# Kernel tuning notes

Measured on AMD Instinct MI355X. Metric: run time of the kernel, lower is better.

The kernel has to match this reference:

```python
import jax, jax.numpy as jnp
import numpy as np

KERNEL_SIZE = 7
STRIDE = 1
PADDING = 3
DILATION = 1
PAD_MODE = 1  # 1 -> reflection pad, 0 -> zero pad (SAN convention)


def setup_inputs() -> dict:
    key = jax.random.key(0)
    x = jax.random.normal(key, (8, 64, 56, 56), dtype=jnp.float32)
    return {"input_": x}


def _subtraction(x, k, stride, padding, dilation, pad_mode):
    B, C, H, W = x.shape
    Hout = (H + 2 * padding - dilation * (k - 1) - 1) // stride + 1
    Wout = (W + 2 * padding - dilation * (k - 1) - 1) // stride + 1
    mode = "reflect" if pad_mode == 1 else "constant"
    xp = jnp.pad(x, ((0, 0), (0, 0), (padding, padding), (padding, padding)), mode=mode)
    # center: 1x1 unfold of the UNPADDED input with the same stride -> [B,C,Hout,Wout]
    center = x[:, :, ::stride, ::stride][:, :, :Hout, :Wout]
    # neighborhood: k*k shifted strided views of the padded input (no big im2col copy per-view)
    h_span = (Hout - 1) * stride + 1
    w_span = (Wout - 1) * stride + 1
    patches = []
    for i in range(k):
        for j in range(k):
            patches.append(
                xp[:, :,
                   i * dilation : i * dilation + h_span : stride,
                   j * dilation : j * dilation + w_span : stride]
            )
    nb = jnp.stack(patches, axis=2)  # [B, C, k*k, Hout, Wout]
    out = center[:, :, None, :, :] - nb  # broadcast subtract center vs neighborhood
    return out.reshape(B, C, k * k, Hout * Wout)


def reference(input_):
    return _subtraction(input_, KERNEL_SIZE, STRIDE, PADDING, DILATION, PAD_MODE)
```

## Files before the change

### kernel.cpp

```cpp
#include <hip/hip_runtime.h>

#define HH 56
#define WW 56
#define HWOUT (HH * WW)
#define NBC (8 * 64)
#define NBLK (NBC * 7)
#define NXCD 8
#define CPX (NBLK / NXCD)

typedef float f32x4 __attribute__((ext_vector_type(4)));

__device__ __forceinline__ int refl(int t) {
    t = (t < 0) ? -t : t;
    return (t >= HH) ? (2 * HH - 2 - t) : t;
}

__global__ __launch_bounds__(256) void sub_kernel(const float* __restrict__ x,
                                                  float* __restrict__ out) {
    const int bid = blockIdx.x;
    const int blk = (bid % NXCD) * CPX + bid / NXCD;

    const int di = blk % 7;
    const int bc = blk / 7;

    const float* __restrict__ img = x + (size_t)bc * HWOUT;
    float* __restrict__ oplane0 = out + ((size_t)bc * 49 + (size_t)di * 7) * HWOUT;

    for (int q = threadIdx.x; q < HWOUT / 4; q += 256) {
        const int e = q * 4;
        const int h = e / WW;
        const int w = e - h * WW;

        const float* __restrict__ crow = img + h * WW;
        const float* __restrict__ nrow = img + refl(h + di - 3) * WW;

        const f32x4 cen = *reinterpret_cast<const f32x4*>(crow + w);

        float wnd[12];
        {
            const f32x4 lo = *reinterpret_cast<const f32x4*>(nrow + (w == 0 ? 0 : w - 4));
            wnd[0] = lo.x; wnd[1] = lo.y; wnd[2] = lo.z; wnd[3] = lo.w;
        }
        {
            const f32x4 mid = *reinterpret_cast<const f32x4*>(nrow + w);
            wnd[4] = mid.x; wnd[5] = mid.y; wnd[6] = mid.z; wnd[7] = mid.w;
        }
        {
            const f32x4 hi = *reinterpret_cast<const f32x4*>(nrow + (w == 52 ? 48 : w + 4));
            wnd[8] = hi.x; wnd[9] = hi.y; wnd[10] = hi.z; wnd[11] = hi.w;
        }
        if (w == 0) {
            wnd[1] = nrow[3]; wnd[2] = nrow[2]; wnd[3] = nrow[1];
        }
        if (w == 52) {
            wnd[8] = nrow[54]; wnd[9] = nrow[53]; wnd[10] = nrow[52];
        }

        float* __restrict__ op = oplane0 + e;
        #pragma unroll
        for (int djj = 0; djj < 7; ++djj) {
            f32x4 r;
            r.x = cen.x - wnd[djj + 1];
            r.y = cen.y - wnd[djj + 2];
            r.z = cen.z - wnd[djj + 3];
            r.w = cen.w - wnd[djj + 4];
            *reinterpret_cast<f32x4*>(op + (size_t)djj * HWOUT) = r;
        }
    }
}

extern "C" void kernel_launch(void* const* d_in, const int* in_sizes, int n_in,
                              void* d_out, int out_size, void* d_ws, size_t ws_size,
                              hipStream_t stream) {
    const float* x = (const float*)d_in[0];
    float* out = (float*)d_out;
    sub_kernel<<<dim3(NBLK), dim3(256), 0, stream>>>(x, out);
}
```

Baseline: 60.88 us.

## Software-pipeline window loads across unrolled iterations and drop XCD block remap

Replaces the strided loop with a fully unrolled sequence in which the next iteration's input loads are issued before the current iteration's stores, so load latency overlaps with writes. Reflection-edge fixups now reuse values already held in the middle vector instead of issuing extra scalar global loads. The XCD-aware block index remapping is removed, so blocks map directly to planes. This raises register pressure and may change L2 locality across XCDs.

```diff
diff --git a/kernel.cpp b/kernel.cpp
--- a/kernel.cpp
+++ b/kernel.cpp
@@ -3,10 +3,7 @@
 #define HH 56
 #define WW 56
 #define HWOUT (HH * WW)
-#define NBC (8 * 64)
-#define NBLK (NBC * 7)
-#define NXCD 8
-#define CPX (NBLK / NXCD)
+#define NBLK (8 * 64 * 7)
 
 typedef float f32x4 __attribute__((ext_vector_type(4)));
 
@@ -15,58 +12,66 @@
     return (t >= HH) ? (2 * HH - 2 - t) : t;
 }
 
+__device__ __forceinline__ void load_win(const float* __restrict__ img, int di, int q,
+                                         f32x4& cen, f32x4& lo, f32x4& mid, f32x4& hi,
+                                         int& w_out) {
+    const int e = q * 4;
+    const int h = e / WW;
+    const int w = e - h * WW;
+    const float* crow = img + h * WW;
+    const float* nrow = img + refl(h + di - 3) * WW;
+    cen = *reinterpret_cast<const f32x4*>(crow + w);
+    lo  = *reinterpret_cast<const f32x4*>(nrow + (w == 0 ? 0 : w - 4));
+    mid = *reinterpret_cast<const f32x4*>(nrow + w);
+    hi  = *reinterpret_cast<const f32x4*>(nrow + (w == 52 ? 48 : w + 4));
+    w_out = w;
+}
+
+__device__ __forceinline__ void finish(float* __restrict__ oplane0, int q, int w,
+                                       f32x4 cen, f32x4 lo, f32x4 mid, f32x4 hi) {
+    float wnd[12];
+    wnd[0] = lo.x;  wnd[1] = lo.y;  wnd[2] = lo.z;  wnd[3] = lo.w;
+    wnd[4] = mid.x; wnd[5] = mid.y; wnd[6] = mid.z; wnd[7] = mid.w;
+    wnd[8] = hi.x;  wnd[9] = hi.y;  wnd[10] = hi.z; wnd[11] = hi.w;
+    if (w == 0)  { wnd[1] = mid.w; wnd[2] = mid.z; wnd[3] = mid.y; }
+    if (w == 52) { wnd[8] = mid.z; wnd[9] = mid.y; wnd[10] = mid.x; }
+
+    float* __restrict__ op = oplane0 + q * 4;
+    #pragma unroll
+    for (int djj = 0; djj < 7; ++djj) {
+        f32x4 r;
+        r.x = cen.x - wnd[djj + 1];
+        r.y = cen.y - wnd[djj + 2];
+        r.z = cen.z - wnd[djj + 3];
+        r.w = cen.w - wnd[djj + 4];
+        *reinterpret_cast<f32x4*>(op + (size_t)djj * HWOUT) = r;
+    }
+}
+
 __global__ __launch_bounds__(256) void sub_kernel(const float* __restrict__ x,
                                                   float* __restrict__ out) {
-    const int bid = blockIdx.x;
-    const int blk = (bid % NXCD) * CPX + bid / NXCD;
-
+    const int blk = blockIdx.x;
     const int di = blk % 7;
     const int bc = blk / 7;
+    const int tid = threadIdx.x;
 
     const float* __restrict__ img = x + (size_t)bc * HWOUT;
     float* __restrict__ oplane0 = out + ((size_t)bc * 49 + (size_t)di * 7) * HWOUT;
 
-    for (int q = threadIdx.x; q < HWOUT / 4; q += 256) {
-        const int e = q * 4;
-        const int h = e / WW;
-        const int w = e - h * WW;
+    f32x4 c0, l0, m0, h0; int w0;
+    f32x4 c1, l1, m1, h1; int w1;
+    f32x4 c2, l2, m2, h2; int w2;
+    f32x4 c3, l3, m3, h3; int w3;
+    const bool tail = (tid < 784 - 768);
 
-        const float* __restrict__ crow = img + h * WW;
-        const float* __restrict__ nrow = img + refl(h + di - 3) * WW;
-
-        const f32x4 cen = *reinterpret_cast<const f32x4*>(crow + w);
-
-        float wnd[12];
-        {
-            const f32x4 lo = *reinterpret_cast<const f32x4*>(nrow + (w == 0 ? 0 : w - 4));
-            wnd[0] = lo.x; wnd[1] = lo.y; wnd[2] = lo.z; wnd[3] = lo.w;
-        }
-        {
-            const f32x4 mid = *reinterpret_cast<const f32x4*>(nrow + w);
-            wnd[4] = mid.x; wnd[5] = mid.y; wnd[6] = mid.z; wnd[7] = mid.w;
-        }
-        {
-            const f32x4 hi = *reinterpret_cast<const f32x4*>(nrow + (w == 52 ? 48 : w + 4));
-            wnd[8] = hi.x; wnd[9] = hi.y; wnd[10] = hi.z; wnd[11] = hi.w;
-        }
-        if (w == 0) {
-            wnd[1] = nrow[3]; wnd[2] = nrow[2]; wnd[3] = nrow[1];
-        }
-        if (w == 52) {
-            wnd[8] = nrow[54]; wnd[9] = nrow[53]; wnd[10] = nrow[52];
-        }
-
-        float* __restrict__ op = oplane0 + e;
-        #pragma unroll
-        for (int djj = 0; djj < 7; ++djj) {
-            f32x4 r;
-            r.x = cen.x - wnd[djj + 1];
-            r.y = cen.y - wnd[djj + 2];
-            r.z = cen.z - wnd[djj + 3];
-            r.w = cen.w - wnd[djj + 4];
-            *reinterpret_cast<f32x4*>(op + (size_t)djj * HWOUT) = r;
-        }
-    }
+    load_win(img, di, tid,       c0, l0, m0, h0, w0);
+    load_win(img, di, tid + 256, c1, l1, m1, h1, w1);
+    finish(oplane0, tid, w0, c0, l0, m0, h0);
+    load_win(img, di, tid + 512, c2, l2, m2, h2, w2);
+    finish(oplane0, tid + 256, w1, c1, l1, m1, h1);
+    if (tail) load_win(img, di, tid + 768, c3, l3, m3, h3, w3);
+    finish(oplane0, tid + 512, w2, c2, l2, m2, h2);
+    if (tail) finish(oplane0, tid + 768, w3, c3, l3, m3, h3);
 }
 
 extern "C" void kernel_launch(void* const* d_in, const int* in_sizes, int n_in,
```

After: 57.60 us. 1.06x faster.

## Stage each channel plane in LDS and loop all row offsets per block

Applied to the files above, without the earlier changes.

Launches one block per (batch, channel) plane instead of seven, loading the plane into shared memory once and reusing it for all seven row offsets. Reflection edge values are taken from the already loaded middle vector rather than extra loads. This aims to cut redundant global reads of the input, but it reduces the grid to 512 blocks and drops the XCD-aware block remapping, which may lower occupancy and store throughput for a write-bound kernel.

```diff
diff --git a/kernel.cpp b/kernel.cpp
--- a/kernel.cpp
+++ b/kernel.cpp
@@ -4,9 +4,6 @@
 #define WW 56
 #define HWOUT (HH * WW)
 #define NBC (8 * 64)
-#define NBLK (NBC * 7)
-#define NXCD 8
-#define CPX (NBLK / NXCD)
 
 typedef float f32x4 __attribute__((ext_vector_type(4)));
 
@@ -17,54 +14,51 @@
 
 __global__ __launch_bounds__(256) void sub_kernel(const float* __restrict__ x,
                                                   float* __restrict__ out) {
-    const int bid = blockIdx.x;
-    const int blk = (bid % NXCD) * CPX + bid / NXCD;
+    __shared__ float img[HWOUT];
+    const int bc = blockIdx.x;
+    const int tid = threadIdx.x;
 
-    const int di = blk % 7;
-    const int bc = blk / 7;
+    const float* __restrict__ gimg = x + (size_t)bc * HWOUT;
+    for (int q = tid; q < HWOUT / 4; q += 256) {
+        *reinterpret_cast<f32x4*>(&img[q * 4]) =
+            *reinterpret_cast<const f32x4*>(gimg + q * 4);
+    }
+    __syncthreads();
 
-    const float* __restrict__ img = x + (size_t)bc * HWOUT;
-    float* __restrict__ oplane0 = out + ((size_t)bc * 49 + (size_t)di * 7) * HWOUT;
+    float* __restrict__ obase = out + (size_t)bc * 49 * HWOUT;
 
-    for (int q = threadIdx.x; q < HWOUT / 4; q += 256) {
-        const int e = q * 4;
-        const int h = e / WW;
-        const int w = e - h * WW;
+    for (int di = 0; di < 7; ++di) {
+        float* __restrict__ oplane0 = obase + (size_t)di * 7 * HWOUT;
+        for (int q = tid; q < HWOUT / 4; q += 256) {
+            const int e = q * 4;
+            const int h = e / WW;
+            const int w = e - h * WW;
 
-        const float* __restrict__ crow = img + h * WW;
-        const float* __restrict__ nrow = img + refl(h + di - 3) * WW;
+            const float* crow = &img[h * WW];
+            const float* nrow = &img[refl(h + di - 3) * WW];
 
-        const f32x4 cen = *reinterpret_cast<const f32x4*>(crow + w);
+            const f32x4 cen = *reinterpret_cast<const f32x4*>(crow + w);
+            const f32x4 lo  = *reinterpret_cast<const f32x4*>(nrow + (w == 0  ? 0  : w - 4));
+            const f32x4 mid = *reinterpret_cast<const f32x4*>(nrow + w);
+            const f32x4 hi  = *reinterpret_cast<const f32x4*>(nrow + (w == 52 ? 48 : w + 4));
 
-        float wnd[12];
-        {
-            const f32x4 lo = *reinterpret_cast<const f32x4*>(nrow + (w == 0 ? 0 : w - 4));
-            wnd[0] = lo.x; wnd[1] = lo.y; wnd[2] = lo.z; wnd[3] = lo.w;
-        }
-        {
-            const f32x4 mid = *reinterpret_cast<const f32x4*>(nrow + w);
+            float wnd[12];
+            wnd[0] = lo.x;  wnd[1] = lo.y;  wnd[2] = lo.z;  wnd[3] = lo.w;
             wnd[4] = mid.x; wnd[5] = mid.y; wnd[6] = mid.z; wnd[7] = mid.w;
-        }
-        {
-            const f32x4 hi = *reinterpret_cast<const f32x4*>(nrow + (w == 52 ? 48 : w + 4));
-            wnd[8] = hi.x; wnd[9] = hi.y; wnd[10] = hi.z; wnd[11] = hi.w;
-        }
-        if (w == 0) {
-            wnd[1] = nrow[3]; wnd[2] = nrow[2]; wnd[3] = nrow[1];
-        }
-        if (w == 52) {
-            wnd[8] = nrow[54]; wnd[9] = nrow[53]; wnd[10] = nrow[52];
-        }
+            wnd[8] = hi.x;  wnd[9] = hi.y;  wnd[10] = hi.z; wnd[11] = hi.w;
+            if (w == 0)  { wnd[1] = mid.w; wnd[2] = mid.z; wnd[3] = mid.y; }
+            if (w == 52) { wnd[8] = mid.z; wnd[9] = mid.y; wnd[10] = mid.x; }
 
-        float* __restrict__ op = oplane0 + e;
-        #pragma unroll
-        for (int djj = 0; djj < 7; ++djj) {
-            f32x4 r;
-            r.x = cen.x - wnd[djj + 1];
-            r.y = cen.y - wnd[djj + 2];
-            r.z = cen.z - wnd[djj + 3];
-            r.w = cen.w - wnd[djj + 4];
-            *reinterpret_cast<f32x4*>(op + (size_t)djj * HWOUT) = r;
+            float* op = oplane0 + e;
+            #pragma unroll
+            for (int djj = 0; djj < 7; ++djj) {
+                f32x4 r;
+                r.x = cen.x - wnd[djj + 1];
+                r.y = cen.y - wnd[djj + 2];
+                r.z = cen.z - wnd[djj + 3];
+                r.w = cen.w - wnd[djj + 4];
+                *reinterpret_cast<f32x4*>(op + (size_t)djj * HWOUT) = r;
+            }
         }
     }
 }
@@ -74,5 +68,5 @@
                               hipStream_t stream) {
     const float* x = (const float*)d_in[0];
     float* out = (float*)d_out;
-    sub_kernel<<<dim3(NBLK), dim3(256), 0, stream>>>(x, out);
+    sub_kernel<<<dim3(NBC), dim3(256), 0, stream>>>(x, out);
 }
```

New measurement: 59.50 us. -2.3%, faster.
